# Optimization experiments

Hardware: AMD Instinct MI355X
Metric: run time of the kernel (lower is better)

Reference implementation:

```python
import jax, jax.numpy as jnp
import numpy as np

B, T_AUX, UP = 4, 75, 110
N_AUX, N_Q, HID, SKIP = 54, 256, 192, 256
K, AUX_K = 6, 3
DIL_FACTS = [0, 1, 2] * 3  # dilation_depth=3, dilation_repeat=3
T = T_AUX * UP - 1  # 8249


def conv1d(x, w, b, dil=1, pad=(0, 0)):
    # x: (B,C,T), w: (O,I,K) torch Conv1d layout
    if pad != (0, 0):
        x = jnp.pad(x, ((0, 0), (0, 0), pad))
    y = jax.lax.conv_general_dilated(x, w, (1,), 'VALID', rhs_dilation=(dil,),
                                     dimension_numbers=('NCH', 'OIH', 'NCH'))
    return y + b[None, :, None]


def setup_inputs() -> dict:
    key = jax.random.key(0)
    ks = jax.random.split(key, 24)
    s = 0.05
    inp = {
        'audio': jax.random.normal(ks[0], (B, N_Q, T), jnp.float32),
        'aux': jax.random.normal(ks[1], (B, N_AUX, T_AUX), jnp.float32),
        'scale_in_w': jax.random.normal(ks[2], (N_AUX, N_AUX, 1), jnp.float32) * s,
        'scale_in_b': jax.random.normal(ks[3], (N_AUX,), jnp.float32) * s,
        'aux0_w': jax.random.normal(ks[4], (N_AUX * 3, N_AUX, AUX_K), jnp.float32) * s,
        'aux0_b': jax.random.normal(ks[5], (N_AUX * 3,), jnp.float32) * s,
        'aux1_w': jax.random.normal(ks[6], (N_AUX * 9, N_AUX * 3, AUX_K), jnp.float32) * s,
        'aux1_b': jax.random.normal(ks[7], (N_AUX * 9,), jnp.float32) * s,
        'up_w': jax.random.normal(ks[8], (UP,), jnp.float32) * s,
        'up_b': jax.random.normal(ks[9], (), jnp.float32) * s,
        'causal_w': jax.random.normal(ks[10], (HID, N_Q, K), jnp.float32) * s,
        'causal_b': jax.random.normal(ks[11], (HID,), jnp.float32) * s,
        'inx_w': jax.random.normal(ks[12], (9, 2 * HID, N_AUX * 9, 1), jnp.float32) * s,
        'inx_b': jax.random.normal(ks[13], (9, 2 * HID), jnp.float32) * s,
        'dilh_w': jax.random.normal(ks[14], (9, 2 * HID, HID, K), jnp.float32) * s,
        'dilh_b': jax.random.normal(ks[15], (9, 2 * HID), jnp.float32) * s,
        'skip_w': jax.random.normal(ks[16], (9, SKIP, HID, 1), jnp.float32) * s,
        'skip_b': jax.random.normal(ks[17], (9, SKIP), jnp.float32) * s,
        'out1_w': jax.random.normal(ks[18], (N_Q, SKIP, 1), jnp.float32) * s,
        'out1_b': jax.random.normal(ks[19], (N_Q,), jnp.float32) * s,
        'out2_w': jax.random.normal(ks[20], (N_Q, N_Q, 1), jnp.float32) * s,
        'out2_b': jax.random.normal(ks[21], (N_Q,), jnp.float32) * s,
    }
    return inp


def reference(audio, aux, scale_in_w, scale_in_b, aux0_w, aux0_b, aux1_w, aux1_b,
              up_w, up_b, causal_w, causal_b, inx_w, inx_b, dilh_w, dilh_b,
              skip_w, skip_b, out1_w, out1_b, out2_w, out2_b):
    # conditioning path: scale_in -> two-sided dilated convs -> deconv upsample
    a = conv1d(aux, scale_in_w, scale_in_b)
    a = conv1d(a, aux0_w, aux0_b, dil=1, pad=(1, 1))      # k=3, dil=1, same length
    a = conv1d(a, aux1_w, aux1_b, dil=3, pad=(3, 3))      # k=3, dil=3, same length
    b_, c_, t_ = a.shape
    x = (a[:, :, :, None] * up_w).reshape(b_, c_, t_ * UP) + up_b  # ConvTranspose2d(1,1,(1,UP))
    x = x[:, :, 1:]  # (B, 486, T)
    # audio path: causal conv (left pad k-1) + softsign
    h = jax.nn.soft_sign(conv1d(audio, causal_w, causal_b, dil=1, pad=(K - 1, 0)))
    sum_out = None
    for l, d in enumerate(DIL_FACTS):
        dil = K ** d
        lpad = dil * (K - 1)  # k**(d+1) - k**d
        xh = conv1d(x, inx_w[l], inx_b[l]) * conv1d(h, dilh_w[l], dilh_b[l], dil=dil, pad=(lpad, 0))
        z = jax.nn.sigmoid(xh[:, :HID])
        h = (1.0 - z) * jnp.tanh(xh[:, HID:]) + z * h
        skip = conv1d(h, skip_w[l], skip_b[l])
        sum_out = skip if sum_out is None else sum_out + skip
    out = conv1d(jax.nn.relu(sum_out), out1_w, out1_b)
    out = conv1d(jax.nn.relu(out), out2_w, out2_b)
    return out.transpose(0, 2, 1)  # (B, T, n_quantize)
```

## Files before the change

kernel.cpp:

```cpp
#include <hip/hip_runtime.h>

#define TLEN 8249
#define TPAD 8320
#define NTILES 130
#define NB 4
#define NAUX 54
#define NQ 256
#define HID 192
#define NSKIP 256
#define KW 6
#define UPF 110
#define TAUX 75
#define PADR 180
#define HROWS (PADR + TPAD)

typedef __attribute__((ext_vector_type(8))) short bf16x8v;
typedef __attribute__((ext_vector_type(4))) float f32x4;

__device__ __forceinline__ unsigned short f2bf(float f) {
  unsigned int u = __float_as_uint(f);
  u += 0x7FFFu + ((u >> 16) & 1u);
  return (unsigned short)(u >> 16);
}

__device__ __forceinline__ f32x4 mfma16(bf16x8v a, bf16x8v b, f32x4 c) {
  return __builtin_amdgcn_mfma_f32_16x16x32_bf16(a, b, c, 0, 0, 0);
}

__global__ void prepack_kernel(
    const float* causal_w, const float* dilh_w, const float* skip_w,
    const float* out1_w, const float* out2_w,
    const float* inx_w, const float* inx_b, const float* up_b,
    unsigned short* pk_causal, unsigned short* pk_dilh, unsigned short* pk_skip,
    unsigned short* pk_out1, unsigned short* pk_out2, float* Cbuf)
{
  int i = blockIdx.x * blockDim.x + threadIdx.x;
  if (i < 9*6*6*24*64*8) {
    int t = i;
    int j = t & 7; t >>= 3;
    int lane = t & 63; t >>= 6;
    int nf = t % 24; t /= 24;
    int kc = t % 6; t /= 6;
    int tap = t % 6; t /= 6;
    int l = t;
    int oc = nf*16 + (lane & 15);
    int ic = kc*32 + ((lane >> 4) << 3) + j;
    pk_dilh[i] = f2bf(dilh_w[((l*384 + oc)*HID + ic)*KW + tap]);
  }
  if (i < 6*8*12*64*8) {
    int t = i;
    int j = t & 7; t >>= 3;
    int lane = t & 63; t >>= 6;
    int nf = t % 12; t /= 12;
    int kc = t % 8; t /= 8;
    int tap = t;
    int oc = nf*16 + (lane & 15);
    int ic = kc*32 + ((lane >> 4) << 3) + j;
    pk_causal[i] = f2bf(causal_w[(oc*NQ + ic)*KW + tap]);
  }
// ... 77 lines not shown
  int co = tid;
  if (co >= 486) return;
  float acc = bias[co];
  for (int c = 0; c < 162; c++)
    #pragma unroll
    for (int k = 0; k < 3; k++)
      acc += w[(co*162 + c)*3 + k] * s[k][c];
  a3[(b*486 + co)*TAUX + q] = acc;
}

__global__ void g_kernel(const float* a3, const float* inx_w, float* G) {
  __shared__ float s[486][15];
  int q0 = blockIdx.x * 15, b = blockIdx.y, l = blockIdx.z;
  int tid = threadIdx.x;
  for (int i = tid; i < 486*15; i += 384) {
    int c = i / 15, qq = i % 15;
    s[c][qq] = a3[(b*486 + c)*TAUX + q0 + qq];
  }
  __syncthreads();
  int oc = tid;
  float acc[15];
  #pragma unroll
  for (int qq = 0; qq < 15; qq++) acc[qq] = 0.f;
  const float* wrow = inx_w + (l*384 + oc)*486;
  for (int c = 0; c < 486; c++) {
    float w = wrow[c];
    #pragma unroll
    for (int qq = 0; qq < 15; qq++) acc[qq] += w * s[c][qq];
  }
  for (int qq = 0; qq < 15; qq++)
    G[((size_t)(l*NB + b)*TAUX + q0 + qq)*384 + oc] = acc[qq];
}

__global__ __launch_bounds__(256, 2)
void causal_kernel(const float* audio, const unsigned short* pk, const float* cb,
                   unsigned short* hbf)
{
  __shared__ __align__(16) unsigned short sA[72*264];
  int b = blockIdx.y, t0 = blockIdx.x*64, tid = threadIdx.x;
  int wv = tid >> 6, lane = tid & 63, lanelo = lane & 15, lanehi = lane >> 4;

  for (int i = tid; i < 72*256; i += 256) {
    int ic = i / 72, tt = i % 72;
    int t = t0 - 5 + tt;
    float v = (t >= 0 && t < TLEN) ? audio[(size_t)(b*NQ + ic)*TLEN + t] : 0.f;
    sA[tt*264 + ic] = f2bf(v);
  }
  __syncthreads();

  f32x4 acc[4][3];
  f32x4 z4 = {0.f, 0.f, 0.f, 0.f};
  #pragma unroll
  for (int m = 0; m < 4; m++)
    #pragma unroll
    for (int i = 0; i < 3; i++) acc[m][i] = z4;

  for (int tap = 0; tap < 6; tap++) {
    for (int kc = 0; kc < 8; kc++) {
      bf16x8v A[4];
      int ko = kc*32 + (lanehi << 3);
      #pragma unroll
      for (int m = 0; m < 4; m++)
        A[m] = *(const bf16x8v*)&sA[(m*16 + lanelo + tap)*264 + ko];
      #pragma unroll
      for (int i = 0; i < 3; i++) {
        int nf = wv*3 + i;
        bf16x8v Bf = *(const bf16x8v*)&pk[(size_t)((((tap*8) + kc)*12 + nf)*64 + lane)*8];
        #pragma unroll
        for (int m = 0; m < 4; m++) acc[m][i] = mfma16(A[m], Bf, acc[m][i]);
      }
    }
  }
// ... 3 lines not shown
  for (int m = 0; m < 4; m++)
    #pragma unroll
    for (int i = 0; i < 3; i++) {
      int oc = (wv*3 + i)*16 + lanelo;
      float bias = cb[oc];
      #pragma unroll
      for (int r = 0; r < 4; r++) {
        float v = acc[m][i][r] + bias;
        hv[m][i][r] = f2bf(v / (1.f + fabsf(v)));
      }
    }
  __syncthreads();
  #pragma unroll
  for (int m = 0; m < 4; m++)
    #pragma unroll
    for (int i = 0; i < 3; i++) {
      int oc = (wv*3 + i)*16 + lanelo;
      int cbh = oc >> 3, jh = oc & 7;
      #pragma unroll
      for (int r = 0; r < 4; r++) {
        int tl = m*16 + (lanehi << 2) + r;
        sA[tl*192 + ((cbh ^ (tl&7))<<3) + jh] = hv[m][i][r];
      }
    }
  __syncthreads();
  #pragma unroll
  for (int j = 0; j < 6; j++) {
    int c = tid + j*256, row = c/24, cbk = c%24;
    uint4 v = *(const uint4*)&sA[row*192 + ((cbk ^ (row&7))<<3)];
    *(uint4*)&hbf[(size_t)(b*HROWS + t0 + row + PADR)*HID + cbk*8] = v;
  }
}

__global__ __launch_bounds__(256, 3)
void layer_kernel(int dil,
                  const unsigned short* __restrict__ hin,
                  unsigned short* __restrict__ hout,
                  const unsigned short* __restrict__ pk_dilh_l,
                  const float* __restrict__ dilh_b_l,
                  const float* __restrict__ Gl, const float* __restrict__ Cl,
                  const float* __restrict__ up_w)
{
  __shared__ __align__(16) unsigned short hs[2][64*192];
  int b = blockIdx.y, t0 = blockIdx.x*64, tid = threadIdx.x;
  int wv = tid >> 6, lane = tid & 63, lanelo = lane & 15, lanehi = lane >> 4;

  const size_t hbase = (size_t)b * HROWS * HID;
  int rowbase0 = t0 - 5*dil + PADR;

  f32x4 accz[4][3], acct[4][3];
  f32x4 z4 = {0.f, 0.f, 0.f, 0.f};
  #pragma unroll
  for (int m = 0; m < 4; m++)
    #pragma unroll
    for (int i = 0; i < 3; i++) { accz[m][i] = z4; acct[m][i] = z4; }

  const unsigned short* holdbuf;
  int holdoff;
  unsigned short* flat = &hs[0][0];

  if (dil != 36) {
    int W = 64 + 5*dil;
    for (int c = tid; c < W*24; c += 256) {
      int row = c/24, cbk = c%24;
      uint4 v = *(const uint4*)&hin[hbase + (size_t)(rowbase0+row)*HID + cbk*8];
      *(uint4*)&flat[row*192 + ((cbk ^ (row&7))<<3)] = v;
    }
    __syncthreads();
    for (int tap = 0; tap < 6; tap++) {
      #pragma unroll
      for (int kc = 0; kc < 6; kc++) {
        bf16x8v A[4];
        #pragma unroll
        for (int m = 0; m < 4; m++) {
          int r = m*16 + lanelo + tap*dil;
          int cbk = kc*4 + lanehi;
          A[m] = *(const bf16x8v*)&flat[r*192 + ((cbk ^ (r&7))<<3)];
        }
        #pragma unroll
        for (int i = 0; i < 3; i++) {
          const unsigned short* bp =
              &pk_dilh_l[(size_t)(((tap*6 + kc)*24 + wv*3 + i)*64 + lane)*8];
          bf16x8v Bz = *(const bf16x8v*)bp;
          bf16x8v Bt = *(const bf16x8v*)(bp + 12*512);
          #pragma unroll
          for (int m = 0; m < 4; m++) {
            accz[m][i] = mfma16(A[m], Bz, accz[m][i]);
            acct[m][i] = mfma16(A[m], Bt, acct[m][i]);
          }
        }
      }
    }
    holdbuf = flat; holdoff = 5*dil;
  } else {
    uint4 st[6];
    #pragma unroll
    for (int j = 0; j < 6; j++) {
      int c = tid + j*256, row = c/24, cbk = c%24;
      st[j] = *(const uint4*)&hin[hbase + (size_t)(rowbase0+row)*HID + cbk*8];
    }
    #pragma unroll
    for (int j = 0; j < 6; j++) {
      int c = tid + j*256, row = c/24, cbk = c%24;
      *(uint4*)&hs[0][row*192 + ((cbk ^ (row&7))<<3)] = st[j];
    }
    for (int tap = 0; tap < 6; tap++) {
      __syncthreads();
      if (tap < 5) {
        int rb = rowbase0 + (tap+1)*36;
        #pragma unroll
        for (int j = 0; j < 6; j++) {
          int c = tid + j*256, row = c/24, cbk = c%24;
          st[j] = *(const uint4*)&hin[hbase + (size_t)(rb+row)*HID + cbk*8];
        }
      }
      const unsigned short* bufc = hs[tap & 1];
      #pragma unroll
      for (int kc = 0; kc < 6; kc++) {
        bf16x8v A[4];
        #pragma unroll
        for (int m = 0; m < 4; m++) {
          int r = m*16 + lanelo;
          int cbk = kc*4 + lanehi;
          A[m] = *(const bf16x8v*)&bufc[r*192 + ((cbk ^ (r&7))<<3)];
        }
        #pragma unroll
        for (int i = 0; i < 3; i++) {
          const unsigned short* bp =
              &pk_dilh_l[(size_t)(((tap*6 + kc)*24 + wv*3 + i)*64 + lane)*8];
          bf16x8v Bz = *(const bf16x8v*)bp;
          bf16x8v Bt = *(const bf16x8v*)(bp + 12*512);
          #pragma unroll
          for (int m = 0; m < 4; m++) {
            accz[m][i] = mfma16(A[m], Bz, accz[m][i]);
            acct[m][i] = mfma16(A[m], Bt, acct[m][i]);
          }
        }
      }
      if (tap < 5) {
        unsigned short* bufn = hs[(tap+1) & 1];
        #pragma unroll
        for (int j = 0; j < 6; j++) {
          int c = tid + j*256, row = c/24, cbk = c%24;
          *(uint4*)&bufn[row*192 + ((cbk ^ (row&7))<<3)] = st[j];
        }
      }
    }
    holdbuf = &hs[1][0]; holdoff = 0;
  }

  float izc[3], itc[3], bzc[3], btc[3];
  #pragma unroll
  for (int i = 0; i < 3; i++) {
    int ocz = (wv*3 + i)*16 + lanelo;
    izc[i] = Cl[ocz];       itc[i] = Cl[192 + ocz];
    bzc[i] = dilh_b_l[ocz]; btc[i] = dilh_b_l[192 + ocz];
  }
  unsigned short hnv[4][4][3];
  #pragma unroll
  for (int m = 0; m < 4; m++) {
    #pragma unroll
    for (int r = 0; r < 4; r++) {
      int tl = m*16 + (lanehi << 2) + r;
      int t = t0 + tl;
      int hr = tl + holdoff;
      int tp1 = t + 1;
      int q = tp1 / UPF; if (q > TAUX - 1) q = TAUX - 1;
      int ui = tp1 - q*UPF; if (ui > UPF - 1) ui = UPF - 1;
      float u = up_w[ui];
      const float* Gb = Gl + (size_t)(b*TAUX + q)*384;
      #pragma unroll
      for (int i = 0; i < 3; i++) {
        int ocz = (wv*3 + i)*16 + lanelo;
        float iz = u*Gb[ocz]       + izc[i];
        float it = u*Gb[192 + ocz] + itc[i];
        float xz = (accz[m][i][r] + bzc[i]) * iz;
        float xt = (acct[m][i][r] + btc[i]) * it;
        float z  = 1.f / (1.f + __expf(-xz));
        float e2 = __expf(2.f*xt);
        float th = 1.f - 2.f/(e2 + 1.f);
        int cbh = ocz >> 3, jh = ocz & 7;
        unsigned short hob = holdbuf[hr*192 + ((cbh ^ (hr&7))<<3) + jh];
        float hold = __uint_as_float(((unsigned int)hob) << 16);
        hnv[m][r][i] = f2bf((1.f - z)*th + z*hold);
      }
    }
  }
  __syncthreads();
  #pragma unroll
  for (int m = 0; m < 4; m++) {
    #pragma unroll
    for (int r = 0; r < 4; r++) {
      int tl = m*16 + (lanehi << 2) + r;
      #pragma unroll
      for (int i = 0; i < 3; i++) {
        int ocz = (wv*3 + i)*16 + lanelo;
        int cbh = ocz >> 3, jh = ocz & 7;
        flat[tl*192 + ((cbh ^ (tl&7))<<3) + jh] = hnv[m][r][i];
      }
    }
  }
  __syncthreads();
  #pragma unroll
  for (int j = 0; j < 6; j++) {
    int c = tid + j*256, row = c/24, cbk = c%24;
    uint4 v = *(const uint4*)&flat[row*192 + ((cbk ^ (row&7))<<3)];
    *(uint4*)&hout[hbase + (size_t)(t0 + row + PADR)*HID + cbk*8] = v;
  }
}

__global__ __launch_bounds__(256, 3)
void skipsum_kernel(const unsigned short* __restrict__ h_all,
                    const unsigned short* __restrict__ pk_skip,
                    const float* __restrict__ skip_b,
                    unsigned short* __restrict__ sbuf)
{
  __shared__ __align__(16) unsigned short ss[2][64*192];
  int b = blockIdx.y, t0 = blockIdx.x*64, tid = threadIdx.x;
  int wv = tid >> 6, lane = tid & 63, lanelo = lane & 15, lanehi = lane >> 4;
  const size_t HS = (size_t)NB * HROWS * HID;

  auto hsrc = [&](int l) {
    int slab = (l == 8) ? 0 : (l + 1);
    return h_all + (size_t)slab*HS + (size_t)b*HROWS*HID + (size_t)(t0 + PADR)*HID;
  };

  uint4 st[6];
  {
    const unsigned short* src = hsrc(0);
    #pragma unroll
    for (int j = 0; j < 6; j++) {
      int c = tid + j*256, row = c/24, cbk = c%24;
      st[j] = *(const uint4*)&src[(size_t)row*HID + cbk*8];
    }
    #pragma unroll
    for (int j = 0; j < 6; j++) {
      int c = tid + j*256, row = c/24, cbk = c%24;
      *(uint4*)&ss[0][row*192 + ((cbk ^ (row&7))<<3)] = st[j];
    }
  }

  f32x4 acc[4][4];
  f32x4 z4 = {0.f, 0.f, 0.f, 0.f};
  #pragma unroll
  for (int m = 0; m < 4; m++)
    #pragma unroll
    for (int i = 0; i < 4; i++) acc[m][i] = z4;

  for (int l = 0; l < 9; l++) {
    __syncthreads();
    if (l < 8) {
      const unsigned short* src = hsrc(l + 1);
      #pragma unroll
      for (int j = 0; j < 6; j++) {
        int c = tid + j*256, row = c/24, cbk = c%24;
        st[j] = *(const uint4*)&src[(size_t)row*HID + cbk*8];
      }
    }
    const unsigned short* bufc = ss[l & 1];
    #pragma unroll
    for (int kc = 0; kc < 6; kc++) {
      bf16x8v A[4];
      #pragma unroll
      for (int m = 0; m < 4; m++) {
        int r = m*16 + lanelo;
        int cbk = kc*4 + lanehi;
        A[m] = *(const bf16x8v*)&bufc[r*192 + ((cbk ^ (r&7))<<3)];
      }
      #pragma unroll
      for (int i = 0; i < 4; i++) {
        bf16x8v Bf = *(const bf16x8v*)
            &pk_skip[(size_t)(((l*6 + kc)*16 + wv*4 + i)*64 + lane)*8];
        #pragma unroll
        for (int m = 0; m < 4; m++) acc[m][i] = mfma16(A[m], Bf, acc[m][i]);
      }
    }
    if (l < 8) {
      unsigned short* bufn = ss[(l+1) & 1];
      #pragma unroll
      for (int j = 0; j < 6; j++) {
        int c = tid + j*256, row = c/24, cbk = c%24;
        *(uint4*)&bufn[row*192 + ((cbk ^ (row&7))<<3)] = st[j];
      }
    }
  }
  __syncthreads();

  unsigned short* tile = &ss[0][0];
  #pragma unroll
  for (int i = 0; i < 4; i++) {
    int sc = (wv*4 + i)*16 + lanelo;
    float bias = 0.f;
    #pragma unroll
    for (int l = 0; l < 9; l++) bias += skip_b[l*NSKIP + sc];
    int cbh = sc >> 3, jh = sc & 7;
    #pragma unroll
    for (int m = 0; m < 4; m++) {
      #pragma unroll
      for (int r = 0; r < 4; r++) {
        int tl = m*16 + (lanehi << 2) + r;
        float v = acc[m][i][r] + bias;
        tile[tl*256 + ((cbh ^ (tl&7))<<3) + jh] = f2bf(fmaxf(v, 0.f));
      }
    }
  }
  __syncthreads();
  #pragma unroll
  for (int j = 0; j < 8; j++) {
    int c = tid + j*256, row = c >> 5, cbk = c & 31;
    uint4 v = *(const uint4*)&tile[row*256 + ((cbk ^ (row&7))<<3)];
    *(uint4*)&sbuf[(size_t)(b*TPAD + t0 + row)*NSKIP + cbk*8] = v;
  }
}

__global__ __launch_bounds__(256, 2)
void out_kernel(const unsigned short* sbuf, const unsigned short* pk1, const float* b1,
                const unsigned short* pk2, const float* b2, float* dout)
{
  __shared__ __align__(16) unsigned short s0[64*264];
  __shared__ __align__(16) float so2[32*260];
  int b = blockIdx.y, t0 = blockIdx.x*64, tid = threadIdx.x;
  int wv = tid >> 6, lane = tid & 63, lanelo = lane & 15, lanehi = lane >> 4;
  f32x4 z4 = {0.f, 0.f, 0.f, 0.f};

  for (int i = tid; i < 64*32; i += 256) {
    int r = i >> 5, cbk = i & 31;
    *(uint4*)&s0[r*264 + cbk*8] =
        *(const uint4*)&sbuf[(size_t)(b*TPAD + t0 + r)*NSKIP + cbk*8];
  }
  __syncthreads();

  f32x4 acc[4][4];
  #pragma unroll
  for (int m = 0; m < 4; m++)
    #pragma unroll
    for (int i = 0; i < 4; i++) acc[m][i] = z4;
  for (int kc = 0; kc < 8; kc++) {
    bf16x8v A[4];
    int ko = kc*32 + (lanehi << 3);
    #pragma unroll
    for (int m = 0; m < 4; m++)
      A[m] = *(const bf16x8v*)&s0[(m*16 + lanelo)*264 + ko];
    #pragma unroll
    for (int i = 0; i < 4; i++) {
      int nf = wv*4 + i;
      bf16x8v Bf = *(const bf16x8v*)&pk1[(size_t)((kc*16 + nf)*64 + lane)*8];
      #pragma unroll
      for (int m = 0; m < 4; m++) acc[m][i] = mfma16(A[m], Bf, acc[m][i]);
    }
  }
  __syncthreads();
  #pragma unroll
  for (int m = 0; m < 4; m++)
    #pragma unroll
// ... 88 lines not shown
  size_t off = 0;
  auto alloc = [&](size_t bytes) -> void* {
    void* p = ws + off;
    off += (bytes + 255) & ~(size_t)255;
    return p;
  };
  unsigned short* pk_causal = (unsigned short*)alloc((size_t)6*8*12*64*8*2);
  unsigned short* pk_dilh   = (unsigned short*)alloc((size_t)9*6*6*24*64*8*2);
  unsigned short* pk_skip   = (unsigned short*)alloc((size_t)9*6*16*64*8*2);
  unsigned short* pk_out1   = (unsigned short*)alloc((size_t)8*16*64*8*2);
  unsigned short* pk_out2   = (unsigned short*)alloc((size_t)8*16*64*8*2);
  float* Cbuf    = (float*)alloc((size_t)9*384*4);
  float* a1      = (float*)alloc((size_t)NB*NAUX*TAUX*4);
  float* a2      = (float*)alloc((size_t)NB*162*TAUX*4);
  float* a3      = (float*)alloc((size_t)NB*486*TAUX*4);
  float* Gbuf    = (float*)alloc((size_t)9*NB*TAUX*384*4);
  const size_t HS = (size_t)NB*HROWS*HID;
  unsigned short* h_all = (unsigned short*)alloc((size_t)9*HS*2);
  unsigned short* sbuf  = (unsigned short*)alloc((size_t)NB*TPAD*NSKIP*2);

  hipLaunchKernelGGL(prepack_kernel, dim3((9*6*6*24*64*8 + 255)/256), dim3(256), 0, stream,
                     causal_w, dilh_w, skip_w, out1_w, out2_w, inx_w, inx_b, up_b,
                     pk_causal, pk_dilh, pk_skip, pk_out1, pk_out2, Cbuf);
  hipLaunchKernelGGL(zpad_kernel, dim3((9*NB*PADR*HID + 255)/256), dim3(256), 0, stream,
                     h_all);
  hipLaunchKernelGGL(aux1_kernel, dim3(TAUX, NB), dim3(64), 0, stream,
                     aux, scale_in_w, scale_in_b, a1);
  hipLaunchKernelGGL(aux2_kernel, dim3(TAUX, NB), dim3(192), 0, stream,
                     a1, aux0_w, aux0_b, a2);
  hipLaunchKernelGGL(aux3_kernel, dim3(TAUX, NB), dim3(512), 0, stream,
                     a2, aux1_w, aux1_b, a3);
  hipLaunchKernelGGL(g_kernel, dim3(5, NB, 9), dim3(384), 0, stream,
                     a3, inx_w, Gbuf);
  hipLaunchKernelGGL(causal_kernel, dim3(NTILES, NB), dim3(256), 0, stream,
                     audio, pk_causal, causal_b, h_all );

  const int dils[9] = {1, 6, 36, 1, 6, 36, 1, 6, 36};
  for (int l = 0; l < 9; l++) {
    const unsigned short* hin = h_all + (size_t)l*HS;
    unsigned short* hout      = (l == 8) ? h_all : h_all + (size_t)(l+1)*HS;
    hipLaunchKernelGGL(layer_kernel, dim3(NTILES, NB), dim3(256), 0, stream,
                       dils[l], hin, hout,
                       pk_dilh + (size_t)l*6*6*24*64*8,
                       dilh_b + (size_t)l*384,
                       Gbuf + (size_t)l*NB*TAUX*384,
                       Cbuf + (size_t)l*384,
                       up_w);
  }

  hipLaunchKernelGGL(skipsum_kernel, dim3(NTILES, NB), dim3(256), 0, stream,
                     h_all, pk_skip, skip_b, sbuf);
  hipLaunchKernelGGL(out_kernel, dim3(NTILES, NB), dim3(256), 0, stream,
                     sbuf, pk_out1, out1_b, pk_out2, out2_b, (float*)d_out);
}
```

Before: 924.2 us.

## Use 128-row tiles with 512 threads for small-dilation layers and skipsum

Small-dilation layers (dil 1 and 6) move to a new kernel that processes 128 time steps per block with 8 waves split 2x4 over time and channel. This amortises the dilation halo and the weight fetches over twice as many rows. The dil-36 path becomes its own specialised kernel. Skipsum also moves to 128-row tiles with 512 threads, using a single staging buffer and writing its output in two halves. The cost is fewer blocks (260 instead of 520), which may lower occupancy and parallelism.

```diff
diff --git a/kernel.cpp b/kernel.cpp
--- a/kernel.cpp
+++ b/kernel.cpp
@@ -3,6 +3,7 @@
 #define TLEN 8249
 #define TPAD 8320
 #define NTILES 130
+#define NTILES2 65
 #define NB 4
 #define NAUX 54
 #define NQ 256
@@ -243,21 +244,137 @@
   }
 }
 
+__global__ __launch_bounds__(512, 2)
+void layer_u_kernel(int dil,
+                    const unsigned short* __restrict__ hin,
+                    unsigned short* __restrict__ hout,
+                    const unsigned short* __restrict__ pk_dilh_l,
+                    const float* __restrict__ dilh_b_l,
+                    const float* __restrict__ Gl, const float* __restrict__ Cl,
+                    const float* __restrict__ up_w)
+{
+  __shared__ __align__(16) unsigned short flat[158*192];
+  int b = blockIdx.y, t0 = blockIdx.x*128, tid = threadIdx.x;
+  int wv = tid >> 6, lane = tid & 63, lanelo = lane & 15, lanehi = lane >> 4;
+  int mwv = wv >> 2, nwv = wv & 3;
+
+  const size_t hbase = (size_t)b * HROWS * HID;
+  int rowbase0 = t0 - 5*dil + PADR;
+  int W = 128 + 5*dil;
+
+  for (int c = tid; c < W*24; c += 512) {
+    int row = c/24, cbk = c%24;
+    uint4 v = *(const uint4*)&hin[hbase + (size_t)(rowbase0+row)*HID + cbk*8];
+    *(uint4*)&flat[row*192 + ((cbk ^ (row&7))<<3)] = v;
+  }
+  __syncthreads();
+
+  f32x4 accz[4][3], acct[4][3];
+  f32x4 z4 = {0.f, 0.f, 0.f, 0.f};
+  #pragma unroll
+  for (int m = 0; m < 4; m++)
+    #pragma unroll
+    for (int i = 0; i < 3; i++) { accz[m][i] = z4; acct[m][i] = z4; }
+
+  for (int tap = 0; tap < 6; tap++) {
+    #pragma unroll
+    for (int kc = 0; kc < 6; kc++) {
+      bf16x8v A[4];
+      int cbk = kc*4 + lanehi;
+      #pragma unroll
+      for (int m = 0; m < 4; m++) {
+        int r = mwv*64 + m*16 + lanelo + tap*dil;
+        A[m] = *(const bf16x8v*)&flat[r*192 + ((cbk ^ (r&7))<<3)];
+      }
+      #pragma unroll
+      for (int i = 0; i < 3; i++) {
+        const unsigned short* bp =
+            &pk_dilh_l[(size_t)(((tap*6 + kc)*24 + nwv*3 + i)*64 + lane)*8];
+        bf16x8v Bz = *(const bf16x8v*)bp;
+        bf16x8v Bt = *(const bf16x8v*)(bp + 12*512);
+        #pragma unroll
+        for (int m = 0; m < 4; m++) {
+          accz[m][i] = mfma16(A[m], Bz, accz[m][i]);
+          acct[m][i] = mfma16(A[m], Bt, acct[m][i]);
+        }
+      }
+    }
+  }
+
+  float izc[3], itc[3], bzc[3], btc[3];
+  #pragma unroll
+  for (int i = 0; i < 3; i++) {
+    int ocz = (nwv*3 + i)*16 + lanelo;
+    izc[i] = Cl[ocz];       itc[i] = Cl[192 + ocz];
+    bzc[i] = dilh_b_l[ocz]; btc[i] = dilh_b_l[192 + ocz];
+  }
+  unsigned short hnv[4][4][3];
+  #pragma unroll
+  for (int m = 0; m < 4; m++) {
+    #pragma unroll
+    for (int r = 0; r < 4; r++) {
+      int tl = mwv*64 + m*16 + (lanehi << 2) + r;
+      int t = t0 + tl;
+      int hr = tl + 5*dil;
+      int tp1 = t + 1;
+      int q = tp1 / UPF; if (q > TAUX - 1) q = TAUX - 1;
+      int ui = tp1 - q*UPF; if (ui > UPF - 1) ui = UPF - 1;
+      float u = up_w[ui];
+      const float* Gb = Gl + (size_t)(b*TAUX + q)*384;
+      #pragma unroll
+      for (int i = 0; i < 3; i++) {
+        int ocz = (nwv*3 + i)*16 + lanelo;
+        float iz = u*Gb[ocz]       + izc[i];
+        float it = u*Gb[192 + ocz] + itc[i];
+        float xz = (accz[m][i][r] + bzc[i]) * iz;
+        float xt = (acct[m][i][r] + btc[i]) * it;
+        float z  = 1.f / (1.f + __expf(-xz));
+        float e2 = __expf(2.f*xt);
+        float th = 1.f - 2.f/(e2 + 1.f);
+        int cbh = ocz >> 3, jh = ocz & 7;
+        unsigned short hob = flat[hr*192 + ((cbh ^ (hr&7))<<3) + jh];
+        float hold = __uint_as_float(((unsigned int)hob) << 16);
+        hnv[m][r][i] = f2bf((1.f - z)*th + z*hold);
+      }
+    }
+  }
+  __syncthreads();
+  #pragma unroll
+  for (int m = 0; m < 4; m++) {
+    #pragma unroll
+    for (int r = 0; r < 4; r++) {
+      int tl = mwv*64 + m*16 + (lanehi << 2) + r;
+      #pragma unroll
+      for (int i = 0; i < 3; i++) {
+        int ocz = (nwv*3 + i)*16 + lanelo;
+        int cbh = ocz >> 3, jh = ocz & 7;
+        flat[tl*192 + ((cbh ^ (tl&7))<<3) + jh] = hnv[m][r][i];
+      }
+    }
+  }
+  __syncthreads();
+  #pragma unroll
+  for (int j = 0; j < 6; j++) {
+    int c = tid + j*512, row = c/24, cbk = c%24;
+    uint4 v = *(const uint4*)&flat[row*192 + ((cbk ^ (row&7))<<3)];
+    *(uint4*)&hout[hbase + (size_t)(t0 + row + PADR)*HID + cbk*8] = v;
+  }
+}
+
 __global__ __launch_bounds__(256, 3)
-void layer_kernel(int dil,
-                  const unsigned short* __restrict__ hin,
-                  unsigned short* __restrict__ hout,
-                  const unsigned short* __restrict__ pk_dilh_l,
-                  const float* __restrict__ dilh_b_l,
-                  const float* __restrict__ Gl, const float* __restrict__ Cl,
-                  const float* __restrict__ up_w)
+void layer_d_kernel(const unsigned short* __restrict__ hin,
+                    unsigned short* __restrict__ hout,
+                    const unsigned short* __restrict__ pk_dilh_l,
+                    const float* __restrict__ dilh_b_l,
+                    const float* __restrict__ Gl, const float* __restrict__ Cl,
+                    const float* __restrict__ up_w)
 {
   __shared__ __align__(16) unsigned short hs[2][64*192];
   int b = blockIdx.y, t0 = blockIdx.x*64, tid = threadIdx.x;
   int wv = tid >> 6, lane = tid & 63, lanelo = lane & 15, lanehi = lane >> 4;
 
   const size_t hbase = (size_t)b * HROWS * HID;
-  int rowbase0 = t0 - 5*dil + PADR;
+  int rowbase0 = t0 - 180 + PADR;
 
   f32x4 accz[4][3], acct[4][3];
   f32x4 z4 = {0.f, 0.f, 0.f, 0.f};
@@ -266,98 +383,58 @@
     #pragma unroll
     for (int i = 0; i < 3; i++) { accz[m][i] = z4; acct[m][i] = z4; }
 
-  const unsigned short* holdbuf;
-  int holdoff;
-  unsigned short* flat = &hs[0][0];
-
-  if (dil != 36) {
-    int W = 64 + 5*dil;
-    for (int c = tid; c < W*24; c += 256) {
-      int row = c/24, cbk = c%24;
-      uint4 v = *(const uint4*)&hin[hbase + (size_t)(rowbase0+row)*HID + cbk*8];
-      *(uint4*)&flat[row*192 + ((cbk ^ (row&7))<<3)] = v;
-    }
+  uint4 st[6];
+  #pragma unroll
+  for (int j = 0; j < 6; j++) {
+    int c = tid + j*256, row = c/24, cbk = c%24;
+    st[j] = *(const uint4*)&hin[hbase + (size_t)(rowbase0+row)*HID + cbk*8];
+  }
+  #pragma unroll
+  for (int j = 0; j < 6; j++) {
+    int c = tid + j*256, row = c/24, cbk = c%24;
+    *(uint4*)&hs[0][row*192 + ((cbk ^ (row&7))<<3)] = st[j];
+  }
+  for (int tap = 0; tap < 6; tap++) {
     __syncthreads();
-    for (int tap = 0; tap < 6; tap++) {
-      #pragma unroll
-      for (int kc = 0; kc < 6; kc++) {
-        bf16x8v A[4];
+    if (tap < 5) {
+      int rb = rowbase0 + (tap+1)*36;
+      #pragma unroll
+      for (int j = 0; j < 6; j++) {
+        int c = tid + j*256, row = c/24, cbk = c%24;
+        st[j] = *(const uint4*)&hin[hbase + (size_t)(rb+row)*HID + cbk*8];
+      }
+    }
+    const unsigned short* bufc = hs[tap & 1];
+    #pragma unroll
+    for (int kc = 0; kc < 6; kc++) {
+      bf16x8v A[4];
+      #pragma unroll
+      for (int m = 0; m < 4; m++) {
+        int r = m*16 + lanelo;
+        int cbk = kc*4 + lanehi;
+        A[m] = *(const bf16x8v*)&bufc[r*192 + ((cbk ^ (r&7))<<3)];
+      }
+      #pragma unroll
+      for (int i = 0; i < 3; i++) {
+        const unsigned short* bp =
+            &pk_dilh_l[(size_t)(((tap*6 + kc)*24 + wv*3 + i)*64 + lane)*8];
+        bf16x8v Bz = *(const bf16x8v*)bp;
+        bf16x8v Bt = *(const bf16x8v*)(bp + 12*512);
         #pragma unroll
         for (int m = 0; m < 4; m++) {
-          int r = m*16 + lanelo + tap*dil;
-          int cbk = kc*4 + lanehi;
-          A[m] = *(const bf16x8v*)&flat[r*192 + ((cbk ^ (r&7))<<3)];
+          accz[m][i] = mfma16(A[m], Bz, accz[m][i]);
+          acct[m][i] = mfma16(A[m], Bt, acct[m][i]);
         }
-        #pragma unroll
-        for (int i = 0; i < 3; i++) {
-          const unsigned short* bp =
-              &pk_dilh_l[(size_t)(((tap*6 + kc)*24 + wv*3 + i)*64 + lane)*8];
-          bf16x8v Bz = *(const bf16x8v*)bp;
-          bf16x8v Bt = *(const bf16x8v*)(bp + 12*512);
-          #pragma unroll
-          for (int m = 0; m < 4; m++) {
-            accz[m][i] = mfma16(A[m], Bz, accz[m][i]);
-            acct[m][i] = mfma16(A[m], Bt, acct[m][i]);
-          }
-        }
-      }
-    }
-    holdbuf = flat; holdoff = 5*dil;
-  } else {
-    uint4 st[6];
-    #pragma unroll
-    for (int j = 0; j < 6; j++) {
-      int c = tid + j*256, row = c/24, cbk = c%24;
-      st[j] = *(const uint4*)&hin[hbase + (size_t)(rowbase0+row)*HID + cbk*8];
-    }
-    #pragma unroll
-    for (int j = 0; j < 6; j++) {
-      int c = tid + j*256, row = c/24, cbk = c%24;
-      *(uint4*)&hs[0][row*192 + ((cbk ^ (row&7))<<3)] = st[j];
-    }
-    for (int tap = 0; tap < 6; tap++) {
-      __syncthreads();
-      if (tap < 5) {
-        int rb = rowbase0 + (tap+1)*36;
-        #pragma unroll
-        for (int j = 0; j < 6; j++) {
-          int c = tid + j*256, row = c/24, cbk = c%24;
-          st[j] = *(const uint4*)&hin[hbase + (size_t)(rb+row)*HID + cbk*8];
-        }
-      }
-      const unsigned short* bufc = hs[tap & 1];
-      #pragma unroll
-      for (int kc = 0; kc < 6; kc++) {
-        bf16x8v A[4];
-        #pragma unroll
-        for (int m = 0; m < 4; m++) {
-          int r = m*16 + lanelo;
-          int cbk = kc*4 + lanehi;
-          A[m] = *(const bf16x8v*)&bufc[r*192 + ((cbk ^ (r&7))<<3)];
-        }
-        #pragma unroll
-        for (int i = 0; i < 3; i++) {
-          const unsigned short* bp =
-              &pk_dilh_l[(size_t)(((tap*6 + kc)*24 + wv*3 + i)*64 + lane)*8];
-          bf16x8v Bz = *(const bf16x8v*)bp;
-          bf16x8v Bt = *(const bf16x8v*)(bp + 12*512);
-          #pragma unroll
-          for (int m = 0; m < 4; m++) {
-            accz[m][i] = mfma16(A[m], Bz, accz[m][i]);
-            acct[m][i] = mfma16(A[m], Bt, acct[m][i]);
-          }
-        }
-      }
-      if (tap < 5) {
-        unsigned short* bufn = hs[(tap+1) & 1];
-        #pragma unroll
-        for (int j = 0; j < 6; j++) {
-          int c = tid + j*256, row = c/24, cbk = c%24;
-          *(uint4*)&bufn[row*192 + ((cbk ^ (row&7))<<3)] = st[j];
-        }
-      }
-    }
-    holdbuf = &hs[1][0]; holdoff = 0;
+      }
+    }
+    if (tap < 5) {
+      unsigned short* bufn = hs[(tap+1) & 1];
+      #pragma unroll
+      for (int j = 0; j < 6; j++) {
+        int c = tid + j*256, row = c/24, cbk = c%24;
+        *(uint4*)&bufn[row*192 + ((cbk ^ (row&7))<<3)] = st[j];
+      }
+    }
   }
 
   float izc[3], itc[3], bzc[3], btc[3];
@@ -374,7 +451,6 @@
     for (int r = 0; r < 4; r++) {
       int tl = m*16 + (lanehi << 2) + r;
       int t = t0 + tl;
-      int hr = tl + holdoff;
       int tp1 = t + 1;
       int q = tp1 / UPF; if (q > TAUX - 1) q = TAUX - 1;
       int ui = tp1 - q*UPF; if (ui > UPF - 1) ui = UPF - 1;
@@ -391,13 +467,14 @@
         float e2 = __expf(2.f*xt);
         float th = 1.f - 2.f/(e2 + 1.f);
         int cbh = ocz >> 3, jh = ocz & 7;
-        unsigned short hob = holdbuf[hr*192 + ((cbh ^ (hr&7))<<3) + jh];
+        unsigned short hob = hs[1][tl*192 + ((cbh ^ (tl&7))<<3) + jh];
         float hold = __uint_as_float(((unsigned int)hob) << 16);
         hnv[m][r][i] = f2bf((1.f - z)*th + z*hold);
       }
     }
   }
   __syncthreads();
+  unsigned short* flat = &hs[0][0];
   #pragma unroll
   for (int m = 0; m < 4; m++) {
     #pragma unroll
@@ -420,15 +497,16 @@
   }
 }
 
-__global__ __launch_bounds__(256, 3)
+__global__ __launch_bounds__(512, 2)
 void skipsum_kernel(const unsigned short* __restrict__ h_all,
                     const unsigned short* __restrict__ pk_skip,
                     const float* __restrict__ skip_b,
                     unsigned short* __restrict__ sbuf)
 {
-  __shared__ __align__(16) unsigned short ss[2][64*192];
-  int b = blockIdx.y, t0 = blockIdx.x*64, tid = threadIdx.x;
+  __shared__ __align__(16) unsigned short ss[128*192];
+  int b = blockIdx.y, t0 = blockIdx.x*128, tid = threadIdx.x;
   int wv = tid >> 6, lane = tid & 63, lanelo = lane & 15, lanehi = lane >> 4;
+  int mwv = wv >> 2, nwv = wv & 3;
   const size_t HS = (size_t)NB * HROWS * HID;
 
   auto hsrc = [&](int l) {
@@ -441,13 +519,13 @@
     const unsigned short* src = hsrc(0);
     #pragma unroll
     for (int j = 0; j < 6; j++) {
-      int c = tid + j*256, row = c/24, cbk = c%24;
+      int c = tid + j*512, row = c/24, cbk = c%24;
       st[j] = *(const uint4*)&src[(size_t)row*HID + cbk*8];
     }
     #pragma unroll
     for (int j = 0; j < 6; j++) {
-      int c = tid + j*256, row = c/24, cbk = c%24;
-      *(uint4*)&ss[0][row*192 + ((cbk ^ (row&7))<<3)] = st[j];
+      int c = tid + j*512, row = c/24, cbk = c%24;
+      *(uint4*)&ss[row*192 + ((cbk ^ (row&7))<<3)] = st[j];
     }
   }
 
@@ -459,68 +537,75 @@
     for (int i = 0; i < 4; i++) acc[m][i] = z4;
 
   for (int l = 0; l < 9; l++) {
+    if (l < 8) {
+      const unsigned short* src = hsrc(l + 1);
+      #pragma unroll
+      for (int j = 0; j < 6; j++) {
+        int c = tid + j*512, row = c/24, cbk = c%24;
+        st[j] = *(const uint4*)&src[(size_t)row*HID + cbk*8];
+      }
+    }
+    __syncthreads();
+    #pragma unroll
+    for (int kc = 0; kc < 6; kc++) {
+      bf16x8v A[4];
+      #pragma unroll
+      for (int m = 0; m < 4; m++) {
+        int r = mwv*64 + m*16 + lanelo;
+        int cbk = kc*4 + lanehi;
+        A[m] = *(const bf16x8v*)&ss[r*192 + ((cbk ^ (r&7))<<3)];
+      }
+      #pragma unroll
+      for (int i = 0; i < 4; i++) {
+        bf16x8v Bf = *(const bf16x8v*)
+            &pk_skip[(size_t)(((l*6 + kc)*16 + nwv*4 + i)*64 + lane)*8];
+        #pragma unroll
+        for (int m = 0; m < 4; m++) acc[m][i] = mfma16(A[m], Bf, acc[m][i]);
+      }
+    }
     __syncthreads();
     if (l < 8) {
-      const unsigned short* src = hsrc(l + 1);
       #pragma unroll
       for (int j = 0; j < 6; j++) {
-        int c = tid + j*256, row = c/24, cbk = c%24;
-        st[j] = *(const uint4*)&src[(size_t)row*HID + cbk*8];
-      }
-    }
-    const unsigned short* bufc = ss[l & 1];
-    #pragma unroll
-    for (int kc = 0; kc < 6; kc++) {
-      bf16x8v A[4];
-      #pragma unroll
-      for (int m = 0; m < 4; m++) {
-        int r = m*16 + lanelo;
-        int cbk = kc*4 + lanehi;
-        A[m] = *(const bf16x8v*)&bufc[r*192 + ((cbk ^ (r&7))<<3)];
-      }
+        int c = tid + j*512, row = c/24, cbk = c%24;
+        *(uint4*)&ss[row*192 + ((cbk ^ (row&7))<<3)] = st[j];
+      }
+    }
+  }
+
+  float biasv[4];
+  #pragma unroll
+  for (int i = 0; i < 4; i++) {
+    int sc = (nwv*4 + i)*16 + lanelo;
+    float bias = 0.f;
+    #pragma unroll
+    for (int l = 0; l < 9; l++) bias += skip_b[l*NSKIP + sc];
+    biasv[i] = bias;
+  }
+  #pragma unroll
+  for (int p = 0; p < 2; p++) {
+    if (mwv == p) {
       #pragma unroll
       for (int i = 0; i < 4; i++) {
-        bf16x8v Bf = *(const bf16x8v*)
-            &pk_skip[(size_t)(((l*6 + kc)*16 + wv*4 + i)*64 + lane)*8];
+        int sc = (nwv*4 + i)*16 + lanelo;
         #pragma unroll
-        for (int m = 0; m < 4; m++) acc[m][i] = mfma16(A[m], Bf, acc[m][i]);
-      }
-    }
-    if (l < 8) {
-      unsigned short* bufn = ss[(l+1) & 1];
-      #pragma unroll
-      for (int j = 0; j < 6; j++) {
-        int c = tid + j*256, row = c/24, cbk = c%24;
-        *(uint4*)&bufn[row*192 + ((cbk ^ (row&7))<<3)] = st[j];
-      }
-    }
-  }
-  __syncthreads();
-
-  unsigned short* tile = &ss[0][0];
-  #pragma unroll
-  for (int i = 0; i < 4; i++) {
-    int sc = (wv*4 + i)*16 + lanelo;
-    float bias = 0.f;
-    #pragma unroll
-    for (int l = 0; l < 9; l++) bias += skip_b[l*NSKIP + sc];
-    int cbh = sc >> 3, jh = sc & 7;
-    #pragma unroll
-    for (int m = 0; m < 4; m++) {
-      #pragma unroll
-      for (int r = 0; r < 4; r++) {
-        int tl = m*16 + (lanehi << 2) + r;
-        float v = acc[m][i][r] + bias;
-        tile[tl*256 + ((cbh ^ (tl&7))<<3) + jh] = f2bf(fmaxf(v, 0.f));
-      }
-    }
-  }
-  __syncthreads();
-  #pragma unroll
-  for (int j = 0; j < 8; j++) {
-    int c = tid + j*256, row = c >> 5, cbk = c & 31;
-    uint4 v = *(const uint4*)&tile[row*256 + ((cbk ^ (row&7))<<3)];
-    *(uint4*)&sbuf[(size_t)(b*TPAD + t0 + row)*NSKIP + cbk*8] = v;
+        for (int m = 0; m < 4; m++) {
+          #pragma unroll
+          for (int r = 0; r < 4; r++) {
+            int lr = m*16 + (lanehi << 2) + r;
+            ss[lr*264 + sc] = f2bf(fmaxf(acc[m][i][r] + biasv[i], 0.f));
+          }
+        }
+      }
+    }
+    __syncthreads();
+    #pragma unroll
+    for (int j = 0; j < 4; j++) {
+      int c = tid + j*512, row = c >> 5, cbk = c & 31;
+      uint4 v = *(const uint4*)&ss[row*264 + cbk*8];
+      *(uint4*)&sbuf[(size_t)(b*TPAD + t0 + p*64 + row)*NSKIP + cbk*8] = v;
+    }
+    __syncthreads();
   }
 }
 
@@ -692,16 +777,26 @@
   for (int l = 0; l < 9; l++) {
     const unsigned short* hin = h_all + (size_t)l*HS;
     unsigned short* hout      = (l == 8) ? h_all : h_all + (size_t)(l+1)*HS;
-    hipLaunchKernelGGL(layer_kernel, dim3(NTILES, NB), dim3(256), 0, stream,
-                       dils[l], hin, hout,
-                       pk_dilh + (size_t)l*6*6*24*64*8,
-                       dilh_b + (size_t)l*384,
-                       Gbuf + (size_t)l*NB*TAUX*384,
-                       Cbuf + (size_t)l*384,
-                       up_w);
-  }
-
-  hipLaunchKernelGGL(skipsum_kernel, dim3(NTILES, NB), dim3(256), 0, stream,
+    if (dils[l] == 36) {
+      hipLaunchKernelGGL(layer_d_kernel, dim3(NTILES, NB), dim3(256), 0, stream,
+                         hin, hout,
+                         pk_dilh + (size_t)l*6*6*24*64*8,
+                         dilh_b + (size_t)l*384,
+                         Gbuf + (size_t)l*NB*TAUX*384,
+                         Cbuf + (size_t)l*384,
+                         up_w);
+    } else {
+      hipLaunchKernelGGL(layer_u_kernel, dim3(NTILES2, NB), dim3(512), 0, stream,
+                         dils[l], hin, hout,
+                         pk_dilh + (size_t)l*6*6*24*64*8,
+                         dilh_b + (size_t)l*384,
+                         Gbuf + (size_t)l*NB*TAUX*384,
+                         Cbuf + (size_t)l*384,
+                         up_w);
+    }
+  }
+
+  hipLaunchKernelGGL(skipsum_kernel, dim3(NTILES2, NB), dim3(512), 0, stream,
                      h_all, pk_skip, skip_b, sbuf);
   hipLaunchKernelGGL(out_kernel, dim3(NTILES, NB), dim3(256), 0, stream,
                      sbuf, pk_out1, out1_b, pk_out2, out2_b, (float*)d_out);
```

Measured after the change: 1.191 ms. 1.29x slower.

## Split layer kernel by dilation, shrink LDS, swizzle block order, write h directly

Applied to the files above, without the earlier changes.

Splits the layer kernel into a small-dilation variant with a 94-row LDS buffer, launched at 4 blocks per SM, and a dedicated dilation-36 variant with double buffering. The new h values are written straight to global memory instead of being staged through LDS. All tile kernels move to a 1D grid with an XCD-aware block swizzle, and causal_kernel's launch bound is raised to 3. The aim is more occupancy and fewer barriers, at the cost of uncoalesced 2-byte global stores and more register pressure.

```diff
diff --git a/kernel.cpp b/kernel.cpp
--- a/kernel.cpp
+++ b/kernel.cpp
@@ -3,6 +3,7 @@
 #define TLEN 8249
 #define TPAD 8320
 #define NTILES 130
+#define NBLK 520
 #define NB 4
 #define NAUX 54
 #define NQ 256
@@ -25,6 +26,10 @@
 
 __device__ __forceinline__ f32x4 mfma16(bf16x8v a, bf16x8v b, f32x4 c) {
   return __builtin_amdgcn_mfma_f32_16x16x32_bf16(a, b, c, 0, 0, 0);
+}
+
+__device__ __forceinline__ int swz520(int bid) {
+  return (bid & 7) * 65 + (bid >> 3);
 }
 
 __global__ void prepack_kernel(
@@ -168,12 +173,13 @@
     G[((size_t)(l*NB + b)*TAUX + q0 + qq)*384 + oc] = acc[qq];
 }
 
-__global__ __launch_bounds__(256, 2)
+__global__ __launch_bounds__(256, 3)
 void causal_kernel(const float* audio, const unsigned short* pk, const float* cb,
                    unsigned short* hbf)
 {
   __shared__ __align__(16) unsigned short sA[72*264];
-  int b = blockIdx.y, t0 = blockIdx.x*64, tid = threadIdx.x;
+  int wg = swz520(blockIdx.x);
+  int b = wg / NTILES, t0 = (wg % NTILES)*64, tid = threadIdx.x;
   int wv = tid >> 6, lane = tid & 63, lanelo = lane & 15, lanehi = lane >> 4;
 
   for (int i = tid; i < 72*256; i += 256) {
@@ -243,21 +249,30 @@
   }
 }
 
-__global__ __launch_bounds__(256, 3)
-void layer_kernel(int dil,
-                  const unsigned short* __restrict__ hin,
-                  unsigned short* __restrict__ hout,
-                  const unsigned short* __restrict__ pk_dilh_l,
-                  const float* __restrict__ dilh_b_l,
-                  const float* __restrict__ Gl, const float* __restrict__ Cl,
-                  const float* __restrict__ up_w)
+__global__ __launch_bounds__(256, 4)
+void layer_u_kernel(int dil,
+                    const unsigned short* __restrict__ hin,
+                    unsigned short* __restrict__ hout,
+                    const unsigned short* __restrict__ pk_dilh_l,
+                    const float* __restrict__ dilh_b_l,
+                    const float* __restrict__ Gl, const float* __restrict__ Cl,
+                    const float* __restrict__ up_w)
 {
-  __shared__ __align__(16) unsigned short hs[2][64*192];
-  int b = blockIdx.y, t0 = blockIdx.x*64, tid = threadIdx.x;
+  __shared__ __align__(16) unsigned short flat[94*192];
+  int wg = swz520(blockIdx.x);
+  int b = wg / NTILES, t0 = (wg % NTILES)*64, tid = threadIdx.x;
   int wv = tid >> 6, lane = tid & 63, lanelo = lane & 15, lanehi = lane >> 4;
 
   const size_t hbase = (size_t)b * HROWS * HID;
   int rowbase0 = t0 - 5*dil + PADR;
+  int W = 64 + 5*dil;
+
+  for (int c = tid; c < W*24; c += 256) {
+    int row = c/24, cbk = c%24;
+    uint4 v = *(const uint4*)&hin[hbase + (size_t)(rowbase0+row)*HID + cbk*8];
+    *(uint4*)&flat[row*192 + ((cbk ^ (row&7))<<3)] = v;
+  }
+  __syncthreads();
 
   f32x4 accz[4][3], acct[4][3];
   f32x4 z4 = {0.f, 0.f, 0.f, 0.f};
@@ -266,98 +281,29 @@
     #pragma unroll
     for (int i = 0; i < 3; i++) { accz[m][i] = z4; acct[m][i] = z4; }
 
-  const unsigned short* holdbuf;
-  int holdoff;
-  unsigned short* flat = &hs[0][0];
-
-  if (dil != 36) {
-    int W = 64 + 5*dil;
-    for (int c = tid; c < W*24; c += 256) {
-      int row = c/24, cbk = c%24;
-      uint4 v = *(const uint4*)&hin[hbase + (size_t)(rowbase0+row)*HID + cbk*8];
-      *(uint4*)&flat[row*192 + ((cbk ^ (row&7))<<3)] = v;
-    }
-    __syncthreads();
-    for (int tap = 0; tap < 6; tap++) {
-      #pragma unroll
-      for (int kc = 0; kc < 6; kc++) {
-        bf16x8v A[4];
+  for (int tap = 0; tap < 6; tap++) {
+    #pragma unroll
+    for (int kc = 0; kc < 6; kc++) {
+      bf16x8v A[4];
+      int cbk = kc*4 + lanehi;
+      #pragma unroll
+      for (int m = 0; m < 4; m++) {
+        int r = m*16 + lanelo + tap*dil;
+        A[m] = *(const bf16x8v*)&flat[r*192 + ((cbk ^ (r&7))<<3)];
+      }
+      #pragma unroll
+      for (int i = 0; i < 3; i++) {
+        const unsigned short* bp =
+            &pk_dilh_l[(size_t)(((tap*6 + kc)*24 + wv*3 + i)*64 + lane)*8];
+        bf16x8v Bz = *(const bf16x8v*)bp;
+        bf16x8v Bt = *(const bf16x8v*)(bp + 12*512);
         #pragma unroll
         for (int m = 0; m < 4; m++) {
-          int r = m*16 + lanelo + tap*dil;
-          int cbk = kc*4 + lanehi;
-          A[m] = *(const bf16x8v*)&flat[r*192 + ((cbk ^ (r&7))<<3)];
+          accz[m][i] = mfma16(A[m], Bz, accz[m][i]);
+          acct[m][i] = mfma16(A[m], Bt, acct[m][i]);
         }
-        #pragma unroll
-        for (int i = 0; i < 3; i++) {
-          const unsigned short* bp =
-              &pk_dilh_l[(size_t)(((tap*6 + kc)*24 + wv*3 + i)*64 + lane)*8];
-          bf16x8v Bz = *(const bf16x8v*)bp;
-          bf16x8v Bt = *(const bf16x8v*)(bp + 12*512);
-          #pragma unroll
-          for (int m = 0; m < 4; m++) {
-            accz[m][i] = mfma16(A[m], Bz, accz[m][i]);
-            acct[m][i] = mfma16(A[m], Bt, acct[m][i]);
-          }
-        }
-      }
-    }
-    holdbuf = flat; holdoff = 5*dil;
-  } else {
-    uint4 st[6];
-    #pragma unroll
-    for (int j = 0; j < 6; j++) {
-      int c = tid + j*256, row = c/24, cbk = c%24;
-      st[j] = *(const uint4*)&hin[hbase + (size_t)(rowbase0+row)*HID + cbk*8];
-    }
-    #pragma unroll
-    for (int j = 0; j < 6; j++) {
-      int c = tid + j*256, row = c/24, cbk = c%24;
-      *(uint4*)&hs[0][row*192 + ((cbk ^ (row&7))<<3)] = st[j];
-    }
-    for (int tap = 0; tap < 6; tap++) {
-      __syncthreads();
-      if (tap < 5) {
-        int rb = rowbase0 + (tap+1)*36;
-        #pragma unroll
-        for (int j = 0; j < 6; j++) {
-          int c = tid + j*256, row = c/24, cbk = c%24;
-          st[j] = *(const uint4*)&hin[hbase + (size_t)(rb+row)*HID + cbk*8];
-        }
-      }
-      const unsigned short* bufc = hs[tap & 1];
-      #pragma unroll
-      for (int kc = 0; kc < 6; kc++) {
-        bf16x8v A[4];
-        #pragma unroll
-        for (int m = 0; m < 4; m++) {
-          int r = m*16 + lanelo;
-          int cbk = kc*4 + lanehi;
-          A[m] = *(const bf16x8v*)&bufc[r*192 + ((cbk ^ (r&7))<<3)];
-        }
-        #pragma unroll
-        for (int i = 0; i < 3; i++) {
-          const unsigned short* bp =
-              &pk_dilh_l[(size_t)(((tap*6 + kc)*24 + wv*3 + i)*64 + lane)*8];
-          bf16x8v Bz = *(const bf16x8v*)bp;
-          bf16x8v Bt = *(const bf16x8v*)(bp + 12*512);
-          #pragma unroll
-          for (int m = 0; m < 4; m++) {
-            accz[m][i] = mfma16(A[m], Bz, accz[m][i]);
-            acct[m][i] = mfma16(A[m], Bt, acct[m][i]);
-          }
-        }
-      }
-      if (tap < 5) {
-        unsigned short* bufn = hs[(tap+1) & 1];
-        #pragma unroll
-        for (int j = 0; j < 6; j++) {
-          int c = tid + j*256, row = c/24, cbk = c%24;
-          *(uint4*)&bufn[row*192 + ((cbk ^ (row&7))<<3)] = st[j];
-        }
-      }
-    }
-    holdbuf = &hs[1][0]; holdoff = 0;
+      }
+    }
   }
 
   float izc[3], itc[3], bzc[3], btc[3];
@@ -367,14 +313,13 @@
     izc[i] = Cl[ocz];       itc[i] = Cl[192 + ocz];
     bzc[i] = dilh_b_l[ocz]; btc[i] = dilh_b_l[192 + ocz];
   }
-  unsigned short hnv[4][4][3];
   #pragma unroll
   for (int m = 0; m < 4; m++) {
     #pragma unroll
     for (int r = 0; r < 4; r++) {
       int tl = m*16 + (lanehi << 2) + r;
       int t = t0 + tl;
-      int hr = tl + holdoff;
+      int hr = tl + 5*dil;
       int tp1 = t + 1;
       int q = tp1 / UPF; if (q > TAUX - 1) q = TAUX - 1;
       int ui = tp1 - q*UPF; if (ui > UPF - 1) ui = UPF - 1;
@@ -391,32 +336,127 @@
         float e2 = __expf(2.f*xt);
         float th = 1.f - 2.f/(e2 + 1.f);
         int cbh = ocz >> 3, jh = ocz & 7;
-        unsigned short hob = holdbuf[hr*192 + ((cbh ^ (hr&7))<<3) + jh];
+        unsigned short hob = flat[hr*192 + ((cbh ^ (hr&7))<<3) + jh];
         float hold = __uint_as_float(((unsigned int)hob) << 16);
-        hnv[m][r][i] = f2bf((1.f - z)*th + z*hold);
-      }
-    }
-  }
-  __syncthreads();
+        float hn = (1.f - z)*th + z*hold;
+        hout[hbase + (size_t)(t + PADR)*HID + ocz] = f2bf(hn);
+      }
+    }
+  }
+}
+
+__global__ __launch_bounds__(256, 3)
+void layer_d_kernel(const unsigned short* __restrict__ hin,
+                    unsigned short* __restrict__ hout,
+                    const unsigned short* __restrict__ pk_dilh_l,
+                    const float* __restrict__ dilh_b_l,
+                    const float* __restrict__ Gl, const float* __restrict__ Cl,
+                    const float* __restrict__ up_w)
+{
+  __shared__ __align__(16) unsigned short hs[2][64*192];
+  int wg = swz520(blockIdx.x);
+  int b = wg / NTILES, t0 = (wg % NTILES)*64, tid = threadIdx.x;
+  int wv = tid >> 6, lane = tid & 63, lanelo = lane & 15, lanehi = lane >> 4;
+
+  const size_t hbase = (size_t)b * HROWS * HID;
+  int rowbase0 = t0 - 180 + PADR;
+
+  f32x4 accz[4][3], acct[4][3];
+  f32x4 z4 = {0.f, 0.f, 0.f, 0.f};
+  #pragma unroll
+  for (int m = 0; m < 4; m++)
+    #pragma unroll
+    for (int i = 0; i < 3; i++) { accz[m][i] = z4; acct[m][i] = z4; }
+
+  uint4 st[6];
+  #pragma unroll
+  for (int j = 0; j < 6; j++) {
+    int c = tid + j*256, row = c/24, cbk = c%24;
+    st[j] = *(const uint4*)&hin[hbase + (size_t)(rowbase0+row)*HID + cbk*8];
+  }
+  #pragma unroll
+  for (int j = 0; j < 6; j++) {
+    int c = tid + j*256, row = c/24, cbk = c%24;
+    *(uint4*)&hs[0][row*192 + ((cbk ^ (row&7))<<3)] = st[j];
+  }
+  for (int tap = 0; tap < 6; tap++) {
+    __syncthreads();
+    if (tap < 5) {
+      int rb = rowbase0 + (tap+1)*36;
+      #pragma unroll
+      for (int j = 0; j < 6; j++) {
+        int c = tid + j*256, row = c/24, cbk = c%24;
+        st[j] = *(const uint4*)&hin[hbase + (size_t)(rb+row)*HID + cbk*8];
+      }
+    }
+    const unsigned short* bufc = hs[tap & 1];
+    #pragma unroll
+    for (int kc = 0; kc < 6; kc++) {
+      bf16x8v A[4];
+      #pragma unroll
+      for (int m = 0; m < 4; m++) {
+        int r = m*16 + lanelo;
+        int cbk = kc*4 + lanehi;
+        A[m] = *(const bf16x8v*)&bufc[r*192 + ((cbk ^ (r&7))<<3)];
+      }
+      #pragma unroll
+      for (int i = 0; i < 3; i++) {
+        const unsigned short* bp =
+            &pk_dilh_l[(size_t)(((tap*6 + kc)*24 + wv*3 + i)*64 + lane)*8];
+        bf16x8v Bz = *(const bf16x8v*)bp;
+        bf16x8v Bt = *(const bf16x8v*)(bp + 12*512);
+        #pragma unroll
+        for (int m = 0; m < 4; m++) {
+          accz[m][i] = mfma16(A[m], Bz, accz[m][i]);
+          acct[m][i] = mfma16(A[m], Bt, acct[m][i]);
+        }
+      }
+    }
+    if (tap < 5) {
+      unsigned short* bufn = hs[(tap+1) & 1];
+      #pragma unroll
+      for (int j = 0; j < 6; j++) {
+        int c = tid + j*256, row = c/24, cbk = c%24;
+        *(uint4*)&bufn[row*192 + ((cbk ^ (row&7))<<3)] = st[j];
+      }
+    }
+  }
+
+  float izc[3], itc[3], bzc[3], btc[3];
+  #pragma unroll
+  for (int i = 0; i < 3; i++) {
+    int ocz = (wv*3 + i)*16 + lanelo;
+    izc[i] = Cl[ocz];       itc[i] = Cl[192 + ocz];
+    bzc[i] = dilh_b_l[ocz]; btc[i] = dilh_b_l[192 + ocz];
+  }
   #pragma unroll
   for (int m = 0; m < 4; m++) {
     #pragma unroll
     for (int r = 0; r < 4; r++) {
       int tl = m*16 + (lanehi << 2) + r;
+      int t = t0 + tl;
+      int tp1 = t + 1;
+      int q = tp1 / UPF; if (q > TAUX - 1) q = TAUX - 1;
+      int ui = tp1 - q*UPF; if (ui > UPF - 1) ui = UPF - 1;
+      float u = up_w[ui];
+      const float* Gb = Gl + (size_t)(b*TAUX + q)*384;
       #pragma unroll
       for (int i = 0; i < 3; i++) {
         int ocz = (wv*3 + i)*16 + lanelo;
+        float iz = u*Gb[ocz]       + izc[i];
+        float it = u*Gb[192 + ocz] + itc[i];
+        float xz = (accz[m][i][r] + bzc[i]) * iz;
+        float xt = (acct[m][i][r] + btc[i]) * it;
+        float z  = 1.f / (1.f + __expf(-xz));
+        float e2 = __expf(2.f*xt);
+        float th = 1.f - 2.f/(e2 + 1.f);
         int cbh = ocz >> 3, jh = ocz & 7;
-        flat[tl*192 + ((cbh ^ (tl&7))<<3) + jh] = hnv[m][r][i];
-      }
-    }
-  }
-  __syncthreads();
-  #pragma unroll
-  for (int j = 0; j < 6; j++) {
-    int c = tid + j*256, row = c/24, cbk = c%24;
-    uint4 v = *(const uint4*)&flat[row*192 + ((cbk ^ (row&7))<<3)];
-    *(uint4*)&hout[hbase + (size_t)(t0 + row + PADR)*HID + cbk*8] = v;
+        unsigned short hob = hs[1][tl*192 + ((cbh ^ (tl&7))<<3) + jh];
+        float hold = __uint_as_float(((unsigned int)hob) << 16);
+        float hn = (1.f - z)*th + z*hold;
+        hout[hbase + (size_t)(t + PADR)*HID + ocz] = f2bf(hn);
+      }
+    }
   }
 }
 
@@ -427,7 +467,8 @@
                     unsigned short* __restrict__ sbuf)
 {
   __shared__ __align__(16) unsigned short ss[2][64*192];
-  int b = blockIdx.y, t0 = blockIdx.x*64, tid = threadIdx.x;
+  int wg = swz520(blockIdx.x);
+  int b = wg / NTILES, t0 = (wg % NTILES)*64, tid = threadIdx.x;
   int wv = tid >> 6, lane = tid & 63, lanelo = lane & 15, lanehi = lane >> 4;
   const size_t HS = (size_t)NB * HROWS * HID;
 
@@ -530,7 +571,8 @@
 {
   __shared__ __align__(16) unsigned short s0[64*264];
   __shared__ __align__(16) float so2[32*260];
-  int b = blockIdx.y, t0 = blockIdx.x*64, tid = threadIdx.x;
+  int wg = swz520(blockIdx.x);
+  int b = wg / NTILES, t0 = (wg % NTILES)*64, tid = threadIdx.x;
   int wv = tid >> 6, lane = tid & 63, lanelo = lane & 15, lanehi = lane >> 4;
   f32x4 z4 = {0.f, 0.f, 0.f, 0.f};
 
@@ -685,24 +727,34 @@
                      a2, aux1_w, aux1_b, a3);
   hipLaunchKernelGGL(g_kernel, dim3(5, NB, 9), dim3(384), 0, stream,
                      a3, inx_w, Gbuf);
-  hipLaunchKernelGGL(causal_kernel, dim3(NTILES, NB), dim3(256), 0, stream,
+  hipLaunchKernelGGL(causal_kernel, dim3(NBLK), dim3(256), 0, stream,
                      audio, pk_causal, causal_b, h_all );
 
   const int dils[9] = {1, 6, 36, 1, 6, 36, 1, 6, 36};
   for (int l = 0; l < 9; l++) {
     const unsigned short* hin = h_all + (size_t)l*HS;
     unsigned short* hout      = (l == 8) ? h_all : h_all + (size_t)(l+1)*HS;
-    hipLaunchKernelGGL(layer_kernel, dim3(NTILES, NB), dim3(256), 0, stream,
-                       dils[l], hin, hout,
-                       pk_dilh + (size_t)l*6*6*24*64*8,
-                       dilh_b + (size_t)l*384,
-                       Gbuf + (size_t)l*NB*TAUX*384,
-                       Cbuf + (size_t)l*384,
-                       up_w);
-  }
-
-  hipLaunchKernelGGL(skipsum_kernel, dim3(NTILES, NB), dim3(256), 0, stream,
+    if (dils[l] == 36) {
+      hipLaunchKernelGGL(layer_d_kernel, dim3(NBLK), dim3(256), 0, stream,
+                         hin, hout,
+                         pk_dilh + (size_t)l*6*6*24*64*8,
+                         dilh_b + (size_t)l*384,
+                         Gbuf + (size_t)l*NB*TAUX*384,
+                         Cbuf + (size_t)l*384,
+                         up_w);
+    } else {
+      hipLaunchKernelGGL(layer_u_kernel, dim3(NBLK), dim3(256), 0, stream,
+                         dils[l], hin, hout,
+                         pk_dilh + (size_t)l*6*6*24*64*8,
+                         dilh_b + (size_t)l*384,
+                         Gbuf + (size_t)l*NB*TAUX*384,
+                         Cbuf + (size_t)l*384,
+                         up_w);
+    }
+  }
+
+  hipLaunchKernelGGL(skipsum_kernel, dim3(NBLK), dim3(256), 0, stream,
                      h_all, pk_skip, skip_b, sbuf);
-  hipLaunchKernelGGL(out_kernel, dim3(NTILES, NB), dim3(256), 0, stream,
+  hipLaunchKernelGGL(out_kernel, dim3(NBLK), dim3(256), 0, stream,
                      sbuf, pk_out1, out1_b, pk_out2, out2_b, (float*)d_out);
 }
```

New measurement: 1.142 ms. +23.5%, slower.
